# Optimization experiments

Hardware: AMD Instinct MI355X
Metric: run time of the kernel (lower is better)

The kernel has to match this reference:

```python
import math
import jax, jax.numpy as jnp
import numpy as np

B, T, C = 4, 2048, 1024
H = 16
D = C // H  # head dim = 64


def setup_inputs() -> dict:
    key = jax.random.key(0)
    ks = jax.random.split(key, 9)
    s = 0.02
    return {
        "x": jax.random.normal(ks[0], (B, T, C), dtype=jnp.float32),
        "Wq": jax.random.normal(ks[1], (C, C), dtype=jnp.float32) * s,
        "bq": jax.random.normal(ks[2], (C,), dtype=jnp.float32) * s,
        "Wk": jax.random.normal(ks[3], (C, C), dtype=jnp.float32) * s,
        "bk": jax.random.normal(ks[4], (C,), dtype=jnp.float32) * s,
        "Wv": jax.random.normal(ks[5], (C, C), dtype=jnp.float32) * s,
        "bv": jax.random.normal(ks[6], (C,), dtype=jnp.float32) * s,
        "Wo": jax.random.normal(ks[7], (C, C), dtype=jnp.float32) * s,
        "bo": jax.random.normal(ks[8], (C,), dtype=jnp.float32) * s,
    }


def reference(x, Wq, bq, Wk, bk, Wv, bv, Wo, bo):
    # Linear projections (torch Linear: x @ W.T + b), split into heads -> [B,H,T,D]
    def heads(y):
        return y.reshape(B, T, H, D).transpose(0, 2, 1, 3)

    q = heads(x @ Wq.T + bq)
    k = heads(x @ Wk.T + bk)
    v = heads(x @ Wv.T + bv)

    # Full [B,H,T,T] score matrix, scaled by 1/sqrt(D) (no mask, dropout=0 / eval)
    scores = jnp.einsum("bhqd,bhkd->bhqk", q, k) / math.sqrt(D)
    attn = jax.nn.softmax(scores, axis=-1)
    out = jnp.einsum("bhqk,bhkd->bhqd", attn, v)
    out = out.transpose(0, 2, 1, 3).reshape(B, T, C)
    return out @ Wo.T + bo
```

## Files before the change

kernel.cpp:

```cpp
#include <hip/hip_runtime.h>
#include <hip/hip_bf16.h>
#include <stdint.h>

#define Bb 4
#define Tt 2048
#define Cc 1024
#define Hh 16
#define Dd 64

using bf16x8 = __bf16 __attribute__((ext_vector_type(8)));
using f32x4  = float  __attribute__((ext_vector_type(4)));
using f32x2  = float  __attribute__((ext_vector_type(2)));
using f32x16 = float  __attribute__((ext_vector_type(16)));
typedef unsigned short u16;
typedef unsigned int   u32;

#if defined(__has_builtin) && __has_builtin(__builtin_amdgcn_exp2f)
#define EXP2F(x) __builtin_amdgcn_exp2f(x)
#else
#define EXP2F(x) exp2f(x)
#endif

#if defined(__has_builtin) && __has_builtin(__builtin_amdgcn_permlane32_swap)
#define PERMLANE32_SWAP(a, b)                                          \
  do {                                                                 \
    auto _r = __builtin_amdgcn_permlane32_swap((a), (b), false, false);\
    (a) = _r[0]; (b) = _r[1];                                          \
  } while (0)
#else
#define PERMLANE32_SWAP(a, b) \
  asm volatile("v_permlane32_swap_b32 %0, %1" : "+v"(a), "+v"(b))
#endif

__device__ __forceinline__ unsigned cvt_pk_bf16(float lo, float hi) {
  unsigned r;
  asm("v_cvt_pk_bf16_f32 %0, %1, %2" : "=v"(r) : "v"(lo), "v"(hi));
  return r;
}

__device__ __forceinline__ u16 f32_to_bf16(float f) {
  union { float f; unsigned u; } v; v.f = f;
  unsigned r = v.u + 0x7fffu + ((v.u >> 16) & 1u);
  return (u16)(r >> 16);
}

__device__ __forceinline__ void gl2lds16(const u16* g, u16* l) {
  __builtin_amdgcn_global_load_lds(
      (const __attribute__((address_space(1))) u32*)g,
      (__attribute__((address_space(3))) u32*)l, 16, 0, 0);
}

__global__ void cast_f32_to_bf16(const float* __restrict__ in, u16* __restrict__ out, int n) {
  int i = (blockIdx.x * blockDim.x + threadIdx.x) * 4;
  if (i >= n) return;
  float4 v = *reinterpret_cast<const float4*>(in + i);
  ushort4 o;
  o.x = f32_to_bf16(v.x); o.y = f32_to_bf16(v.y);
  o.z = f32_to_bf16(v.z); o.w = f32_to_bf16(v.w);
  *reinterpret_cast<ushort4*>(out + i) = o;
}

__global__ void cast4_f32_to_bf16(const float* __restrict__ w0, const float* __restrict__ w1,
                                  const float* __restrict__ w2, const float* __restrict__ w3,
                                  u16* __restrict__ o0, u16* __restrict__ o1,
                                  u16* __restrict__ o2, u16* __restrict__ o3, int n) {
  const float* in; u16* out;
  switch (blockIdx.y) {
    case 0: in = w0; out = o0; break;
    case 1: in = w1; out = o1; break;
    case 2: in = w2; out = o2; break;
    default: in = w3; out = o3; break;
  }
  int i = (blockIdx.x * blockDim.x + threadIdx.x) * 4;
  if (i >= n) return;
  float4 v = *reinterpret_cast<const float4*>(in + i);
  ushort4 o;
  o.x = f32_to_bf16(v.x); o.y = f32_to_bf16(v.y);
  o.z = f32_to_bf16(v.z); o.w = f32_to_bf16(v.w);
  *reinterpret_cast<ushort4*>(out + i) = o;
}

__global__ __launch_bounds__(256, 2)
void gemm_qkv(const u16* __restrict__ A, const u16* __restrict__ Bqkv,
              const float* __restrict__ bq, const float* __restrict__ bk,
              const float* __restrict__ bv,
              u16* __restrict__ qout, u16* __restrict__ kout, u16* __restrict__ vtout,
              float qscl)
{
  constexpr int K = Cc, BK = 32, LDT = 136;
  __shared__ alignas(16) u16 smem[128 * LDT];
  u16* As = smem;
  u16* Bs = smem + 128 * BK;
  const int tid  = threadIdx.x;
  const int wave = tid >> 6, lane = tid & 63;
  const int row0 = blockIdx.x * 128, col0 = blockIdx.y * 128;
  const int seg  = col0 >> 10;
  const int wm = (wave & 1) * 64, wn = (wave >> 1) * 64;
  const int fr = lane & 15, fk = (lane >> 4) * 8;
  const int srow = lane >> 2, scol = (lane & 3) * 8;

  f32x4 acc[4][4] = {};

  for (int k0 = 0; k0 < K; k0 += BK) {
#pragma unroll
    for (int c = 0; c < 2; ++c) {
      int rg = (wave * 2 + c) * 16;
      gl2lds16(A    + (size_t)(row0 + rg + srow) * K + k0 + scol, &As[rg * BK]);
      gl2lds16(Bqkv + (size_t)(col0 + rg + srow) * K + k0 + scol, &Bs[rg * BK]);
    }
    __syncthreads();
    bf16x8 af[4], bf[4];
#pragma unroll
    for (int i = 0; i < 4; ++i) {
      af[i] = *reinterpret_cast<const bf16x8*>(&As[(wm + i * 16 + fr) * BK + fk]);
      bf[i] = *reinterpret_cast<const bf16x8*>(&Bs[(wn + i * 16 + fr) * BK + fk]);
    }
#pragma unroll
    for (int i = 0; i < 4; ++i)
#pragma unroll
      for (int j = 0; j < 4; ++j)
        acc[i][j] = __builtin_amdgcn_mfma_f32_16x16x32_bf16(af[i], bf[j], acc[i][j], 0, 0, 0);
    __syncthreads();
  }

  const float* bias = (seg == 0) ? bq : ((seg == 1) ? bk : bv);
  const float scale = (seg == 0) ? qscl : 1.0f;
  const int colL0 = col0 & 1023;

  if (seg < 2) {
    u16* outp = (seg == 0) ? qout : kout;
#pragma unroll
    for (int j = 0; j < 4; ++j) {
      int col = colL0 + wn + j * 16 + fr;
      float bvv = bias[col];
#pragma unroll
      for (int i = 0; i < 4; ++i) {
        int rowb = row0 + wm + i * 16 + (lane >> 4) * 4;
#pragma unroll
        for (int r = 0; r < 4; ++r)
          outp[(size_t)(rowb + r) * Cc + col] = f32_to_bf16((acc[i][j][r] + bvv) * scale);
      }
    }
  } else {
#pragma unroll
    for (int j = 0; j < 4; ++j) {
      int lc = wn + j * 16 + fr;
      float bvv = bias[colL0 + lc];
#pragma unroll
      for (int i = 0; i < 4; ++i) {
        int lr = wm + i * 16 + (lane >> 4) * 4;
#pragma unroll
        for (int r = 0; r < 4; ++r)
          smem[lc * LDT + lr + r] = f32_to_bf16(acc[i][j][r] + bvv);
      }
    }
    __syncthreads();
    int lc = tid >> 1, seg2 = tid & 1;
    int col = colL0 + lc;
    int h = col >> 6, d = col & 63;
    int bb = row0 >> 11, t0 = (row0 & 2047) + seg2 * 64;
    u16* dst = vtout + ((size_t)(bb * Hh + h) * Dd + d) * Tt + t0;
    const u16* src = &smem[lc * LDT + seg2 * 64];
#pragma unroll
    for (int g = 0; g < 8; ++g)
      *reinterpret_cast<uint4*>(dst + g * 8) = *reinterpret_cast<const uint4*>(src + g * 8);
  }
}

__global__ __launch_bounds__(256, 2)
void gemm_out(const u16* __restrict__ A, const u16* __restrict__ Bw,
              const float* __restrict__ bias, float* __restrict__ Cout,
              int M, int N, int K)
{
  constexpr int BK = 32;
  __shared__ alignas(16) u16 As[128 * BK];
  __shared__ alignas(16) u16 Bs[128 * BK];
  const int tid  = threadIdx.x;
  const int wave = tid >> 6, lane = tid & 63;
  const int row0 = blockIdx.x * 128, col0 = blockIdx.y * 128;
  const int wm = (wave & 1) * 64, wn = (wave >> 1) * 64;
  const int fr = lane & 15, fk = (lane >> 4) * 8;
  const int srow = lane >> 2, scol = (lane & 3) * 8;

  f32x4 acc[4][4] = {};

  for (int k0 = 0; k0 < K; k0 += BK) {
#pragma unroll
    for (int c = 0; c < 2; ++c) {
      int rg = (wave * 2 + c) * 16;
      gl2lds16(A  + (size_t)(row0 + rg + srow) * K + k0 + scol, &As[rg * BK]);
      gl2lds16(Bw + (size_t)(col0 + rg + srow) * K + k0 + scol, &Bs[rg * BK]);
    }
    __syncthreads();
    bf16x8 af[4], bf[4];
#pragma unroll
    for (int i = 0; i < 4; ++i) {
      af[i] = *reinterpret_cast<const bf16x8*>(&As[(wm + i * 16 + fr) * BK + fk]);
      bf[i] = *reinterpret_cast<const bf16x8*>(&Bs[(wn + i * 16 + fr) * BK + fk]);
    }
#pragma unroll
    for (int i = 0; i < 4; ++i)
#pragma unroll
      for (int j = 0; j < 4; ++j)
        acc[i][j] = __builtin_amdgcn_mfma_f32_16x16x32_bf16(af[i], bf[j], acc[i][j], 0, 0, 0);
    __syncthreads();
  }

#pragma unroll
  for (int j = 0; j < 4; ++j) {
    int col = col0 + wn + j * 16 + fr;
    float bv = bias[col];
#pragma unroll
    for (int i = 0; i < 4; ++i) {
      int rowb = row0 + wm + i * 16 + (lane >> 4) * 4;
#pragma unroll
      for (int r = 0; r < 4; ++r)
        Cout[(size_t)(rowb + r) * N + col] = acc[i][j][r] + bv;
    }
  }
}

__global__ __launch_bounds__(256, 4)
void attn_kernel(const u16* __restrict__ Q, const u16* __restrict__ Kmat,
                 const u16* __restrict__ VT, u16* __restrict__ O) {
  __shared__ alignas(16) unsigned char smem[32768];
  float* OfT = (float*)smem;
  float* Qs  = (float*)(smem + 17408);

  const int tid = threadIdx.x, wave = tid >> 6, lane = tid & 63;
  const int l31 = lane & 31, hi = lane >> 5;
  const int qt = wave >> 1, kh = wave & 1;
  const int bh = blockIdx.x, qt0 = blockIdx.y;
  const int b = bh >> 4, h = bh & 15;
  const size_t base = (size_t)b * Tt * Cc + (size_t)h * Dd;
  const size_t vtb = (size_t)bh * Dd * Tt;

  bf16x8 qb[4];
  {
    const u16* qp = Q + base + (size_t)(qt0 * 64 + qt * 32 + l31) * Cc + hi * 8;
#pragma unroll
    for (int c = 0; c < 4; ++c)
      qb[c] = *reinterpret_cast<const bf16x8*>(qp + c * 16);
  }

  f32x16 Oacc[2] = {};
  f32x2 sacc = {0.f, 0.f};

  const u16* pK = Kmat + base + (size_t)(wave * 16 + (lane >> 3)) * Cc +
                  (((lane & 7) ^ (lane >> 3)) << 3);
  const u16* pV = VT + vtb + (size_t)(wave * 16 + (lane >> 3)) * Tt +
                  (((lane & 7) ^ (lane >> 3)) << 3);

  auto STAGE = [&](int buf, int kt) {
    u16* Kd = (u16*)(smem + (buf << 14)) + wave * 1024;
    u16* Vd = Kd + 4096;
    const u16* pk = pK + (size_t)kt * Cc;
    const u16* pv = pV + kt;
#pragma unroll
    for (int c = 0; c < 2; ++c) {
      gl2lds16(pk + (size_t)(c * 8) * Cc, Kd + c * 512);
      gl2lds16(pv + (size_t)(c * 8) * Tt, Vd + c * 512);
    }
  };

  STAGE(0, 0);
  __syncthreads();

  int cur = 0;
#pragma unroll 1
  for (int t = 0; t < 32; ++t) {
    if (t < 31) STAGE(cur ^ 1, (t + 1) << 6);

    const u16* Ks = (const u16*)(smem + (cur << 14));
    const u16* Vs = Ks + 4096;

    bf16x8 ka[4], vb[2][2];
    const int key = kh * 32 + l31;
#pragma unroll
    for (int c = 0; c < 4; ++c)
      ka[c] = *reinterpret_cast<const bf16x8*>(
          &Ks[key * 64 + ((((c << 1) + hi) ^ (key & 7)) << 3)]);
#pragma unroll
    for (int k0i = 0; k0i < 2; ++k0i)
#pragma unroll
      for (int dh = 0; dh < 2; ++dh) {
        int drow = dh * 32 + l31;
        int ch = kh * 4 + k0i * 2 + hi;
        vb[k0i][dh] = *reinterpret_cast<const bf16x8*>(
            &Vs[drow * 64 + ((ch ^ (drow & 7)) << 3)]);
      }

    __builtin_amdgcn_s_setprio(1);

    f32x16 s = {};
#pragma unroll
    for (int c = 0; c < 4; ++c)
      s = __builtin_amdgcn_mfma_f32_32x32x16_bf16(ka[c], qb[c], s, 0, 0, 0);
    unsigned pk8[8];
#pragma unroll
    for (int i = 0; i < 8; ++i) {
      float p0 = EXP2F(s[2 * i]), p1 = EXP2F(s[2 * i + 1]);
      sacc += (f32x2){p0, p1};
      pk8[i] = cvt_pk_bf16(p0, p1);
    }
    unsigned a0 = pk8[0], a1 = pk8[1], a2 = pk8[2], a3 = pk8[3];
    unsigned b0 = pk8[4], b1 = pk8[5], b2 = pk8[6], b3 = pk8[7];
    PERMLANE32_SWAP(a0, a2);
    PERMLANE32_SWAP(a1, a3);
    PERMLANE32_SWAP(b0, b2);
    PERMLANE32_SWAP(b1, b3);
    union { unsigned u[4]; bf16x8 v; } plo, phi;
    plo.u[0] = a0; plo.u[1] = a1; plo.u[2] = a2; plo.u[3] = a3;
    phi.u[0] = b0; phi.u[1] = b1; phi.u[2] = b2; phi.u[3] = b3;
    Oacc[0] = __builtin_amdgcn_mfma_f32_32x32x16_bf16(plo.v, vb[0][0], Oacc[0], 0, 0, 0);
    Oacc[1] = __builtin_amdgcn_mfma_f32_32x32x16_bf16(plo.v, vb[0][1], Oacc[1], 0, 0, 0);
    Oacc[0] = __builtin_amdgcn_mfma_f32_32x32x16_bf16(phi.v, vb[1][0], Oacc[0], 0, 0, 0);
    Oacc[1] = __builtin_amdgcn_mfma_f32_32x32x16_bf16(phi.v, vb[1][1], Oacc[1], 0, 0, 0);

    __builtin_amdgcn_s_setprio(0);

    __syncthreads();
    cur ^= 1;
  }

  {
    float s = sacc[0] + sacc[1];
    s += __shfl_xor(s, 32, 64);
    if (hi == 0) Qs[wave * 32 + l31] = s;
  }

#pragma unroll
  for (int step = 0; step < 2; ++step) {
    if (kh == step) {
#pragma unroll
      for (int dh = 0; dh < 2; ++dh) {
        int d = dh * 32 + l31;
        float* rowp = &OfT[d * 68 + qt * 32 + hi * 4];
#pragma unroll
        for (int g = 0; g < 4; ++g) {
          f32x4 v;
          v[0] = Oacc[dh][g * 4 + 0]; v[1] = Oacc[dh][g * 4 + 1];
          v[2] = Oacc[dh][g * 4 + 2]; v[3] = Oacc[dh][g * 4 + 3];
          float* dst = rowp + g * 8;
          if (step == 0) *reinterpret_cast<f32x4*>(dst) = v;
          else {
            f32x4 old = *reinterpret_cast<const f32x4*>(dst);
            *reinterpret_cast<f32x4*>(dst) = old + v;
          }
        }
      }
    }
    __syncthreads();
  }

  {
    int q = tid >> 2, dg = tid & 3;
    float qtot = Qs[(q >> 5) * 64 + (q & 31)] + Qs[(q >> 5) * 64 + 32 + (q & 31)];
    float linv = 1.0f / qtot;
    alignas(16) u16 tmp[16];
#pragma unroll
    for (int i = 0; i < 16; ++i)
      tmp[i] = f32_to_bf16(OfT[(dg * 16 + i) * 68 + q] * linv);
    u16* op = O + base + (size_t)(qt0 * 64 + q) * Cc + dg * 16;
    *reinterpret_cast<uint4*>(op)     = *reinterpret_cast<const uint4*>(tmp);
    *reinterpret_cast<uint4*>(op + 8) = *reinterpret_cast<const uint4*>(tmp + 8);
  }
}

extern "C" void kernel_launch(void* const* d_in, const int* in_sizes, int n_in,
                              void* d_out, int out_size, void* d_ws, size_t ws_size,
                              hipStream_t stream) {
  const float* x  = (const float*)d_in[0];
  const float* Wq = (const float*)d_in[1];
  const float* bq = (const float*)d_in[2];
  const float* Wk = (const float*)d_in[3];
  const float* bk = (const float*)d_in[4];
  const float* Wv = (const float*)d_in[5];
  const float* bv = (const float*)d_in[6];
  const float* Wo = (const float*)d_in[7];
  const float* bo = (const float*)d_in[8];

  const size_t NX = (size_t)Bb * Tt * Cc;
  const size_t NW = (size_t)Cc * Cc;

  u16* ws  = (u16*)d_ws;
  u16* xb  = ws;
  u16* wqb = ws + NX;
  u16* wkb = wqb + NW;
  u16* wvb = wkb + NW;
  u16* wob = wvb + NW;
  u16* qb  = wob + NW;
  u16* kb  = qb + NX;
  u16* vtb = kb + NX;
  u16* attnb = xb;

  cast_f32_to_bf16<<<(int)(NX / 4 / 256), 256, 0, stream>>>(x, xb, (int)NX);
  cast4_f32_to_bf16<<<dim3((unsigned)(NW / 4 / 256), 4), 256, 0, stream>>>(
      Wq, Wk, Wv, Wo, wqb, wkb, wvb, wob, (int)NW);

  const float QSCL = 0.125f * 1.44269504f;
  gemm_qkv<<<dim3(64, 24), 256, 0, stream>>>(xb, wqb, bq, bk, bv, qb, kb, vtb, QSCL);

  attn_kernel<<<dim3(Bb * Hh, Tt / 64), 256, 0, stream>>>(qb, kb, vtb, attnb);

  gemm_out<<<dim3(64, 8), 256, 0, stream>>>(attnb, wob, bo, (float*)d_out,
                                            Bb * Tt, Cc, Cc);
}
```

Before: 291.2 us.

## Load K/V tiles directly from global into registers, drop LDS staging, swizzle blocks

The attention kernel no longer stages K and V tiles through double-buffered shared memory with per-iteration barriers. Each wave now reads its K and V fragments straight from global memory into registers, and K loads are software-prefetched one tile ahead. The launch becomes a 1D grid with a block-index swizzle so that neighbouring blocks share the same head, which should improve L2 reuse, and shared memory shrinks. The trade-off is that each wave issues its own, possibly less coalesced global loads, and the two waves sharing keys read duplicate data, so the kernel relies on the cache hierarchy instead of LDS.

```diff
diff --git a/kernel.cpp b/kernel.cpp
--- a/kernel.cpp
+++ b/kernel.cpp
@@ -223,14 +223,16 @@
 __global__ __launch_bounds__(256, 4)
 void attn_kernel(const u16* __restrict__ Q, const u16* __restrict__ Kmat,
                  const u16* __restrict__ VT, u16* __restrict__ O) {
-  __shared__ alignas(16) unsigned char smem[32768];
+  __shared__ alignas(16) unsigned char smem[18432];
   float* OfT = (float*)smem;
   float* Qs  = (float*)(smem + 17408);
 
   const int tid = threadIdx.x, wave = tid >> 6, lane = tid & 63;
   const int l31 = lane & 31, hi = lane >> 5;
   const int qt = wave >> 1, kh = wave & 1;
-  const int bh = blockIdx.x, qt0 = blockIdx.y;
+  const int flat = blockIdx.x;
+  const int swz = (flat & 7) * 256 + (flat >> 3);
+  const int bh = swz >> 5, qt0 = swz & 31;
   const int b = bh >> 4, h = bh & 15;
   const size_t base = (size_t)b * Tt * Cc + (size_t)h * Dd;
   const size_t vtb = (size_t)bh * Dd * Tt;
@@ -246,82 +248,70 @@
   f32x16 Oacc[2] = {};
   f32x2 sacc = {0.f, 0.f};
 
-  const u16* pK = Kmat + base + (size_t)(wave * 16 + (lane >> 3)) * Cc +
-                  (((lane & 7) ^ (lane >> 3)) << 3);
-  const u16* pV = VT + vtb + (size_t)(wave * 16 + (lane >> 3)) * Tt +
-                  (((lane & 7) ^ (lane >> 3)) << 3);
-
-  auto STAGE = [&](int buf, int kt) {
-    u16* Kd = (u16*)(smem + (buf << 14)) + wave * 1024;
-    u16* Vd = Kd + 4096;
-    const u16* pk = pK + (size_t)kt * Cc;
-    const u16* pv = pV + kt;
-#pragma unroll
-    for (int c = 0; c < 2; ++c) {
-      gl2lds16(pk + (size_t)(c * 8) * Cc, Kd + c * 512);
-      gl2lds16(pv + (size_t)(c * 8) * Tt, Vd + c * 512);
-    }
-  };
-
-  STAGE(0, 0);
+  const int koff  = (kh * 32 + l31) * Cc + hi * 8;
+  const int voff0 = l31 * Tt        + kh * 32 + hi * 8;
+  const int voff1 = (32 + l31) * Tt + kh * 32 + hi * 8;
+  const u16* kp = Kmat + base;
+  const u16* vp = VT + vtb;
+
+#define LOADK(T, KA)                                                       \
+  {                                                                        \
+    const u16* kpt = kp + (size_t)(T) * 64 * Cc + koff;                    \
+    KA[0] = *reinterpret_cast<const bf16x8*>(kpt);                         \
+    KA[1] = *reinterpret_cast<const bf16x8*>(kpt + 16);                    \
+    KA[2] = *reinterpret_cast<const bf16x8*>(kpt + 32);                    \
+    KA[3] = *reinterpret_cast<const bf16x8*>(kpt + 48);                    \
+  }
+
+#define BODY(T, KA)                                                        \
+  {                                                                        \
+    const u16* vpt = vp + (T) * 64;                                        \
+    bf16x8 vb00 = *reinterpret_cast<const bf16x8*>(vpt + voff0);           \
+    bf16x8 vb10 = *reinterpret_cast<const bf16x8*>(vpt + voff0 + 16);      \
+    bf16x8 vb01 = *reinterpret_cast<const bf16x8*>(vpt + voff1);           \
+    bf16x8 vb11 = *reinterpret_cast<const bf16x8*>(vpt + voff1 + 16);      \
+    __builtin_amdgcn_s_setprio(1);                                         \
+    f32x16 s = {};                                                         \
+    s = __builtin_amdgcn_mfma_f32_32x32x16_bf16(KA[0], qb[0], s, 0, 0, 0); \
+    s = __builtin_amdgcn_mfma_f32_32x32x16_bf16(KA[1], qb[1], s, 0, 0, 0); \
+    s = __builtin_amdgcn_mfma_f32_32x32x16_bf16(KA[2], qb[2], s, 0, 0, 0); \
+    s = __builtin_amdgcn_mfma_f32_32x32x16_bf16(KA[3], qb[3], s, 0, 0, 0); \
+    unsigned pk8[8];                                                       \
+    _Pragma("unroll")                                                      \
+    for (int i = 0; i < 8; ++i) {                                          \
+      float p0 = EXP2F(s[2 * i]), p1 = EXP2F(s[2 * i + 1]);                \
+      sacc += (f32x2){p0, p1};                                             \
+      pk8[i] = cvt_pk_bf16(p0, p1);                                        \
+    }                                                                      \
+    unsigned a0 = pk8[0], a1 = pk8[1], a2 = pk8[2], a3 = pk8[3];           \
+    unsigned b0 = pk8[4], b1 = pk8[5], b2 = pk8[6], b3 = pk8[7];           \
+    PERMLANE32_SWAP(a0, a2);                                               \
+    PERMLANE32_SWAP(a1, a3);                                               \
+    PERMLANE32_SWAP(b0, b2);                                               \
+    PERMLANE32_SWAP(b1, b3);                                               \
+    union { unsigned u[4]; bf16x8 v; } plo, phi;                           \
+    plo.u[0] = a0; plo.u[1] = a1; plo.u[2] = a2; plo.u[3] = a3;            \
+    phi.u[0] = b0; phi.u[1] = b1; phi.u[2] = b2; phi.u[3] = b3;            \
+    Oacc[0] = __builtin_amdgcn_mfma_f32_32x32x16_bf16(plo.v, vb00, Oacc[0], 0, 0, 0); \
+    Oacc[1] = __builtin_amdgcn_mfma_f32_32x32x16_bf16(plo.v, vb01, Oacc[1], 0, 0, 0); \
+    Oacc[0] = __builtin_amdgcn_mfma_f32_32x32x16_bf16(phi.v, vb10, Oacc[0], 0, 0, 0); \
+    Oacc[1] = __builtin_amdgcn_mfma_f32_32x32x16_bf16(phi.v, vb11, Oacc[1], 0, 0, 0); \
+    __builtin_amdgcn_s_setprio(0);                                         \
+  }
+
+  bf16x8 ka0[4], ka1[4];
+  LOADK(0, ka0);
+#pragma unroll 1
+  for (int t = 0; t < 32; t += 2) {
+    LOADK(t + 1, ka1);
+    BODY(t, ka0);
+    if (t < 30) LOADK(t + 2, ka0);
+    BODY(t + 1, ka1);
+  }
+#undef LOADK
+#undef BODY
+
   __syncthreads();
-
-  int cur = 0;
-#pragma unroll 1
-  for (int t = 0; t < 32; ++t) {
-    if (t < 31) STAGE(cur ^ 1, (t + 1) << 6);
-
-    const u16* Ks = (const u16*)(smem + (cur << 14));
-    const u16* Vs = Ks + 4096;
-
-    bf16x8 ka[4], vb[2][2];
-    const int key = kh * 32 + l31;
-#pragma unroll
-    for (int c = 0; c < 4; ++c)
-      ka[c] = *reinterpret_cast<const bf16x8*>(
-          &Ks[key * 64 + ((((c << 1) + hi) ^ (key & 7)) << 3)]);
-#pragma unroll
-    for (int k0i = 0; k0i < 2; ++k0i)
-#pragma unroll
-      for (int dh = 0; dh < 2; ++dh) {
-        int drow = dh * 32 + l31;
-        int ch = kh * 4 + k0i * 2 + hi;
-        vb[k0i][dh] = *reinterpret_cast<const bf16x8*>(
-            &Vs[drow * 64 + ((ch ^ (drow & 7)) << 3)]);
-      }
-
-    __builtin_amdgcn_s_setprio(1);
-
-    f32x16 s = {};
-#pragma unroll
-    for (int c = 0; c < 4; ++c)
-      s = __builtin_amdgcn_mfma_f32_32x32x16_bf16(ka[c], qb[c], s, 0, 0, 0);
-    unsigned pk8[8];
-#pragma unroll
-    for (int i = 0; i < 8; ++i) {
-      float p0 = EXP2F(s[2 * i]), p1 = EXP2F(s[2 * i + 1]);
-      sacc += (f32x2){p0, p1};
-      pk8[i] = cvt_pk_bf16(p0, p1);
-    }
-    unsigned a0 = pk8[0], a1 = pk8[1], a2 = pk8[2], a3 = pk8[3];
-    unsigned b0 = pk8[4], b1 = pk8[5], b2 = pk8[6], b3 = pk8[7];
-    PERMLANE32_SWAP(a0, a2);
-    PERMLANE32_SWAP(a1, a3);
-    PERMLANE32_SWAP(b0, b2);
-    PERMLANE32_SWAP(b1, b3);
-    union { unsigned u[4]; bf16x8 v; } plo, phi;
-    plo.u[0] = a0; plo.u[1] = a1; plo.u[2] = a2; plo.u[3] = a3;
-    phi.u[0] = b0; phi.u[1] = b1; phi.u[2] = b2; phi.u[3] = b3;
-    Oacc[0] = __builtin_amdgcn_mfma_f32_32x32x16_bf16(plo.v, vb[0][0], Oacc[0], 0, 0, 0);
-    Oacc[1] = __builtin_amdgcn_mfma_f32_32x32x16_bf16(plo.v, vb[0][1], Oacc[1], 0, 0, 0);
-    Oacc[0] = __builtin_amdgcn_mfma_f32_32x32x16_bf16(phi.v, vb[1][0], Oacc[0], 0, 0, 0);
-    Oacc[1] = __builtin_amdgcn_mfma_f32_32x32x16_bf16(phi.v, vb[1][1], Oacc[1], 0, 0, 0);
-
-    __builtin_amdgcn_s_setprio(0);
-
-    __syncthreads();
-    cur ^= 1;
-  }
 
   {
     float s = sacc[0] + sacc[1];
@@ -401,7 +391,7 @@
   const float QSCL = 0.125f * 1.44269504f;
   gemm_qkv<<<dim3(64, 24), 256, 0, stream>>>(xb, wqb, bq, bk, bv, qb, kb, vtb, QSCL);
 
-  attn_kernel<<<dim3(Bb * Hh, Tt / 64), 256, 0, stream>>>(qb, kb, vtb, attnb);
+  attn_kernel<<<dim3(Bb * Hh * (Tt / 64)), 256, 0, stream>>>(qb, kb, vtb, attnb);
 
   gemm_out<<<dim3(64, 8), 256, 0, stream>>>(attnb, wob, bo, (float*)d_out,
                                             Bb * Tt, Cc, Cc);
```

New measurement: 435.7 us. +49.6%, slower.

## Deepen GEMM K-tile to 64 with XOR-swizzled LDS and XCD-aware block mapping

Applied to the files above, without the earlier changes.

Both projection GEMMs now stage K-tiles of 64 instead of 32, halving the number of barrier pairs per output tile. The LDS layout is XOR-swizzled on 16-byte chunks to avoid bank conflicts on the fragment reads. The grid becomes 1D and is remapped so that consecutive blocks on the same XCD cover neighbouring row tiles, improving L2 reuse. The QKV kernel gains an extra barrier before reusing shared memory for the V transpose. LDS use per block doubles in gemm_out.

```diff
diff --git a/kernel.cpp b/kernel.cpp
--- a/kernel.cpp
+++ b/kernel.cpp
@@ -87,39 +87,51 @@
               u16* __restrict__ qout, u16* __restrict__ kout, u16* __restrict__ vtout,
               float qscl)
 {
-  constexpr int K = Cc, BK = 32, LDT = 136;
+  constexpr int K = Cc, BK = 64, LDT = 136;
   __shared__ alignas(16) u16 smem[128 * LDT];
   u16* As = smem;
-  u16* Bs = smem + 128 * BK;
+  u16* Bs = smem + 128 * 64;
   const int tid  = threadIdx.x;
   const int wave = tid >> 6, lane = tid & 63;
-  const int row0 = blockIdx.x * 128, col0 = blockIdx.y * 128;
+  const int lid = blockIdx.x;
+  const int xcd = lid & 7, cch = lid >> 3;
+  const int bx = xcd * 8 + (cch & 7), by = cch >> 3;
+  const int row0 = bx * 128, col0 = by * 128;
   const int seg  = col0 >> 10;
   const int wm = (wave & 1) * 64, wn = (wave >> 1) * 64;
-  const int fr = lane & 15, fk = (lane >> 4) * 8;
-  const int srow = lane >> 2, scol = (lane & 3) * 8;
+  const int fr = lane & 15, qd = lane >> 4;
+  const int srow = lane >> 3;
+  const int scol = ((lane & 7) ^ srow) << 3;
 
   f32x4 acc[4][4] = {};
+  const u16* pA = A    + (size_t)(row0 + wave * 32 + srow) * K + scol;
+  const u16* pB = Bqkv + (size_t)(col0 + wave * 32 + srow) * K + scol;
 
   for (int k0 = 0; k0 < K; k0 += BK) {
 #pragma unroll
-    for (int c = 0; c < 2; ++c) {
-      int rg = (wave * 2 + c) * 16;
-      gl2lds16(A    + (size_t)(row0 + rg + srow) * K + k0 + scol, &As[rg * BK]);
-      gl2lds16(Bqkv + (size_t)(col0 + rg + srow) * K + k0 + scol, &Bs[rg * BK]);
-    }
-    __syncthreads();
-    bf16x8 af[4], bf[4];
-#pragma unroll
-    for (int i = 0; i < 4; ++i) {
-      af[i] = *reinterpret_cast<const bf16x8*>(&As[(wm + i * 16 + fr) * BK + fk]);
-      bf[i] = *reinterpret_cast<const bf16x8*>(&Bs[(wn + i * 16 + fr) * BK + fk]);
-    }
-#pragma unroll
-    for (int i = 0; i < 4; ++i)
-#pragma unroll
-      for (int j = 0; j < 4; ++j)
-        acc[i][j] = __builtin_amdgcn_mfma_f32_16x16x32_bf16(af[i], bf[j], acc[i][j], 0, 0, 0);
+    for (int c = 0; c < 4; ++c) {
+      gl2lds16(pA + (size_t)(c * 8) * K + k0, &As[(wave * 32 + c * 8) * 64]);
+      gl2lds16(pB + (size_t)(c * 8) * K + k0, &Bs[(wave * 32 + c * 8) * 64]);
+    }
+    __syncthreads();
+#pragma unroll
+    for (int kk = 0; kk < 2; ++kk) {
+      bf16x8 af[4], bf[4];
+#pragma unroll
+      for (int i = 0; i < 4; ++i) {
+        int ra = wm + i * 16 + fr;
+        af[i] = *reinterpret_cast<const bf16x8*>(
+            &As[ra * 64 + (((kk * 4 + qd) ^ (ra & 7)) << 3)]);
+        int rb = wn + i * 16 + fr;
+        bf[i] = *reinterpret_cast<const bf16x8*>(
+            &Bs[rb * 64 + (((kk * 4 + qd) ^ (rb & 7)) << 3)]);
+      }
+#pragma unroll
+      for (int i = 0; i < 4; ++i)
+#pragma unroll
+        for (int j = 0; j < 4; ++j)
+          acc[i][j] = __builtin_amdgcn_mfma_f32_16x16x32_bf16(af[i], bf[j], acc[i][j], 0, 0, 0);
+    }
     __syncthreads();
   }
 
@@ -142,6 +154,7 @@
       }
     }
   } else {
+    __syncthreads();
 #pragma unroll
     for (int j = 0; j < 4; ++j) {
       int lc = wn + j * 16 + fr;
@@ -172,37 +185,49 @@
               const float* __restrict__ bias, float* __restrict__ Cout,
               int M, int N, int K)
 {
-  constexpr int BK = 32;
-  __shared__ alignas(16) u16 As[128 * BK];
-  __shared__ alignas(16) u16 Bs[128 * BK];
+  constexpr int BK = 64;
+  __shared__ alignas(16) u16 As[128 * 64];
+  __shared__ alignas(16) u16 Bs[128 * 64];
   const int tid  = threadIdx.x;
   const int wave = tid >> 6, lane = tid & 63;
-  const int row0 = blockIdx.x * 128, col0 = blockIdx.y * 128;
+  const int lid = blockIdx.x;
+  const int xcd = lid & 7, cch = lid >> 3;
+  const int bx = xcd * 8 + (cch & 7), by = cch >> 3;
+  const int row0 = bx * 128, col0 = by * 128;
   const int wm = (wave & 1) * 64, wn = (wave >> 1) * 64;
-  const int fr = lane & 15, fk = (lane >> 4) * 8;
-  const int srow = lane >> 2, scol = (lane & 3) * 8;
+  const int fr = lane & 15, qd = lane >> 4;
+  const int srow = lane >> 3;
+  const int scol = ((lane & 7) ^ srow) << 3;
 
   f32x4 acc[4][4] = {};
+  const u16* pA = A  + (size_t)(row0 + wave * 32 + srow) * K + scol;
+  const u16* pB = Bw + (size_t)(col0 + wave * 32 + srow) * K + scol;
 
   for (int k0 = 0; k0 < K; k0 += BK) {
 #pragma unroll
-    for (int c = 0; c < 2; ++c) {
-      int rg = (wave * 2 + c) * 16;
-      gl2lds16(A  + (size_t)(row0 + rg + srow) * K + k0 + scol, &As[rg * BK]);
-      gl2lds16(Bw + (size_t)(col0 + rg + srow) * K + k0 + scol, &Bs[rg * BK]);
-    }
-    __syncthreads();
-    bf16x8 af[4], bf[4];
-#pragma unroll
-    for (int i = 0; i < 4; ++i) {
-      af[i] = *reinterpret_cast<const bf16x8*>(&As[(wm + i * 16 + fr) * BK + fk]);
-      bf[i] = *reinterpret_cast<const bf16x8*>(&Bs[(wn + i * 16 + fr) * BK + fk]);
-    }
-#pragma unroll
-    for (int i = 0; i < 4; ++i)
-#pragma unroll
-      for (int j = 0; j < 4; ++j)
-        acc[i][j] = __builtin_amdgcn_mfma_f32_16x16x32_bf16(af[i], bf[j], acc[i][j], 0, 0, 0);
+    for (int c = 0; c < 4; ++c) {
+      gl2lds16(pA + (size_t)(c * 8) * K + k0, &As[(wave * 32 + c * 8) * 64]);
+      gl2lds16(pB + (size_t)(c * 8) * K + k0, &Bs[(wave * 32 + c * 8) * 64]);
+    }
+    __syncthreads();
+#pragma unroll
+    for (int kk = 0; kk < 2; ++kk) {
+      bf16x8 af[4], bf[4];
+#pragma unroll
+      for (int i = 0; i < 4; ++i) {
+        int ra = wm + i * 16 + fr;
+        af[i] = *reinterpret_cast<const bf16x8*>(
+            &As[ra * 64 + (((kk * 4 + qd) ^ (ra & 7)) << 3)]);
+        int rb = wn + i * 16 + fr;
+        bf[i] = *reinterpret_cast<const bf16x8*>(
+            &Bs[rb * 64 + (((kk * 4 + qd) ^ (rb & 7)) << 3)]);
+      }
+#pragma unroll
+      for (int i = 0; i < 4; ++i)
+#pragma unroll
+        for (int j = 0; j < 4; ++j)
+          acc[i][j] = __builtin_amdgcn_mfma_f32_16x16x32_bf16(af[i], bf[j], acc[i][j], 0, 0, 0);
+    }
     __syncthreads();
   }
 
@@ -399,10 +424,10 @@
       Wq, Wk, Wv, Wo, wqb, wkb, wvb, wob, (int)NW);
 
   const float QSCL = 0.125f * 1.44269504f;
-  gemm_qkv<<<dim3(64, 24), 256, 0, stream>>>(xb, wqb, bq, bk, bv, qb, kb, vtb, QSCL);
+  gemm_qkv<<<dim3(1536), 256, 0, stream>>>(xb, wqb, bq, bk, bv, qb, kb, vtb, QSCL);
 
   attn_kernel<<<dim3(Bb * Hh, Tt / 64), 256, 0, stream>>>(qb, kb, vtb, attnb);
 
-  gemm_out<<<dim3(64, 8), 256, 0, stream>>>(attnb, wob, bo, (float*)d_out,
-                                            Bb * Tt, Cc, Cc);
-}
+  gemm_out<<<dim3(512), 256, 0, stream>>>(attnb, wob, bo, (float*)d_out,
+                                          Bb * Tt, Cc, Cc);
+}
```

New measurement: 271.3 us. 1.07x faster.

## Replace GEMMs with double-buffered 256x128 swizzled-LDS pipelined kernel and fuse casts

Applied to the files above, without the earlier changes.

Both projection GEMMs now use one kernel with 512 threads, 256x128 tiles, BK=64, XOR-swizzled LDS, and double-buffered global-to-LDS loads. Loads are interleaved with MFMA phases and gated by s_waitcnt, with setprio and an XCD-aware block remap. The two cast kernels are merged into one launch. The aim is to hide global-load latency and cut the per-tile barrier stalls of the old single-buffered 128x128 GEMMs. The cost is more LDS per block (96KB), which limits occupancy, plus fragile hand-written waitcnt/barrier scheduling.

```diff
diff --git a/kernel.cpp b/kernel.cpp
--- a/kernel.cpp
+++ b/kernel.cpp
@@ -50,173 +50,178 @@
       (__attribute__((address_space(3))) u32*)l, 16, 0, 0);
 }
 
-__global__ void cast_f32_to_bf16(const float* __restrict__ in, u16* __restrict__ out, int n) {
-  int i = (blockIdx.x * blockDim.x + threadIdx.x) * 4;
-  if (i >= n) return;
-  float4 v = *reinterpret_cast<const float4*>(in + i);
+__global__ void cast_all(const float* __restrict__ x,
+                         const float* __restrict__ w0, const float* __restrict__ w1,
+                         const float* __restrict__ w2, const float* __restrict__ w3,
+                         u16* __restrict__ out) {
+  size_t e = ((size_t)blockIdx.x * blockDim.x + threadIdx.x) * 4;
+  size_t hi = e >> 20;
+  const float* src;
+  if (hi < 8) {
+    src = x + e;
+  } else {
+    size_t off = e & 1048575u;
+    src = (hi == 8 ? w0 : hi == 9 ? w1 : hi == 10 ? w2 : w3) + off;
+  }
+  float4 v = *reinterpret_cast<const float4*>(src);
   ushort4 o;
   o.x = f32_to_bf16(v.x); o.y = f32_to_bf16(v.y);
   o.z = f32_to_bf16(v.z); o.w = f32_to_bf16(v.w);
-  *reinterpret_cast<ushort4*>(out + i) = o;
-}
-
-__global__ void cast4_f32_to_bf16(const float* __restrict__ w0, const float* __restrict__ w1,
-                                  const float* __restrict__ w2, const float* __restrict__ w3,
-                                  u16* __restrict__ o0, u16* __restrict__ o1,
-                                  u16* __restrict__ o2, u16* __restrict__ o3, int n) {
-  const float* in; u16* out;
-  switch (blockIdx.y) {
-    case 0: in = w0; out = o0; break;
-    case 1: in = w1; out = o1; break;
-    case 2: in = w2; out = o2; break;
-    default: in = w3; out = o3; break;
-  }
-  int i = (blockIdx.x * blockDim.x + threadIdx.x) * 4;
-  if (i >= n) return;
-  float4 v = *reinterpret_cast<const float4*>(in + i);
-  ushort4 o;
-  o.x = f32_to_bf16(v.x); o.y = f32_to_bf16(v.y);
-  o.z = f32_to_bf16(v.z); o.w = f32_to_bf16(v.w);
-  *reinterpret_cast<ushort4*>(out + i) = o;
-}
-
-__global__ __launch_bounds__(256, 2)
-void gemm_qkv(const u16* __restrict__ A, const u16* __restrict__ Bqkv,
-              const float* __restrict__ bq, const float* __restrict__ bk,
-              const float* __restrict__ bv,
-              u16* __restrict__ qout, u16* __restrict__ kout, u16* __restrict__ vtout,
-              float qscl)
+  *reinterpret_cast<ushort4*>(out + e) = o;
+}
+
+__global__ __launch_bounds__(512, 2)
+void gemm8(const u16* __restrict__ A, const u16* __restrict__ Bm,
+           const float* __restrict__ b0, const float* __restrict__ b1,
+           const float* __restrict__ b2,
+           u16* __restrict__ o0, u16* __restrict__ o1, u16* __restrict__ vtout,
+           float* __restrict__ of32, float qscl, int isqkv)
 {
-  constexpr int K = Cc, BK = 32, LDT = 136;
-  __shared__ alignas(16) u16 smem[128 * LDT];
-  u16* As = smem;
-  u16* Bs = smem + 128 * BK;
-  const int tid  = threadIdx.x;
+  constexpr int K = Cc;
+  __shared__ alignas(16) u16 smem16[49152];
+  const int tid = threadIdx.x;
   const int wave = tid >> 6, lane = tid & 63;
-  const int row0 = blockIdx.x * 128, col0 = blockIdx.y * 128;
-  const int seg  = col0 >> 10;
-  const int wm = (wave & 1) * 64, wn = (wave >> 1) * 64;
-  const int fr = lane & 15, fk = (lane >> 4) * 8;
-  const int srow = lane >> 2, scol = (lane & 3) * 8;
+  const int fr = lane & 15, qd = lane >> 4, sw = fr & 7;
+  const int wr = wave >> 1, wc = wave & 1;
+  const int lid = blockIdx.x;
+  const int xcd = lid & 7, idx = lid >> 3;
+  const int bx = xcd * 4 + (idx & 3), by = idx >> 2;
+  const int row0 = bx * 256, col0 = by * 128;
+
+  const u16* pA = A  + (size_t)(row0 + (lane >> 3)) * K + (((lane & 7) ^ (lane >> 3)) << 3);
+  const u16* pB = Bm + (size_t)(col0 + (lane >> 3)) * K + (((lane & 7) ^ (lane >> 3)) << 3);
 
   f32x4 acc[4][4] = {};
-
-  for (int k0 = 0; k0 < K; k0 += BK) {
-#pragma unroll
-    for (int c = 0; c < 2; ++c) {
-      int rg = (wave * 2 + c) * 16;
-      gl2lds16(A    + (size_t)(row0 + rg + srow) * K + k0 + scol, &As[rg * BK]);
-      gl2lds16(Bqkv + (size_t)(col0 + rg + srow) * K + k0 + scol, &Bs[rg * BK]);
+  bf16x8 bfr[4][2];
+
+#define STG_A(BUF, H, T) do {                                              \
+    gl2lds16(pA + (size_t)((H)*128 + wave*16) * K + (T)*64,                \
+             smem16 + (BUF)*24576 + ((H)*128 + wave*16) * 64);             \
+    gl2lds16(pA + (size_t)((H)*128 + wave*16 + 8) * K + (T)*64,            \
+             smem16 + (BUF)*24576 + ((H)*128 + wave*16 + 8) * 64);         \
+  } while (0)
+#define STG_B(BUF, T) do {                                                 \
+    gl2lds16(pB + (size_t)(wave*16) * K + (T)*64,                          \
+             smem16 + (BUF)*24576 + 16384 + (wave*16) * 64);               \
+    gl2lds16(pB + (size_t)(wave*16 + 8) * K + (T)*64,                      \
+             smem16 + (BUF)*24576 + 16384 + (wave*16 + 8) * 64);           \
+  } while (0)
+#define LDA(BUF, Q, KK) (*reinterpret_cast<const bf16x8*>(                 \
+    &smem16[(BUF)*24576 + (wr*64 + (Q)*16 + fr) * 64 + ((((KK)*4 + qd) ^ sw) << 3)]))
+#define LDB(BUF, J, KK) (*reinterpret_cast<const bf16x8*>(                 \
+    &smem16[(BUF)*24576 + 16384 + (wc*64 + (J)*16 + fr) * 64 + ((((KK)*4 + qd) ^ sw) << 3)]))
+#define GATE2 asm volatile("s_waitcnt vmcnt(2)" ::: "memory")
+#define GATE0 asm volatile("s_waitcnt vmcnt(0)" ::: "memory")
+#define GNONE
+#define SBAR do { asm volatile("" ::: "memory");                           \
+    __builtin_amdgcn_s_barrier(); asm volatile("" ::: "memory"); } while (0)
+
+#define PH(Q, BUF, GATE, ...) do {                                         \
+    bf16x8 af0 = LDA(BUF, Q, 0), af1 = LDA(BUF, Q, 1);                     \
+    if ((Q) == 0) {                                                        \
+      bfr[0][0] = LDB(BUF, 0, 0); bfr[0][1] = LDB(BUF, 0, 1);              \
+      bfr[1][0] = LDB(BUF, 1, 0); bfr[1][1] = LDB(BUF, 1, 1);              \
+      bfr[2][0] = LDB(BUF, 2, 0); bfr[2][1] = LDB(BUF, 2, 1);              \
+      bfr[3][0] = LDB(BUF, 3, 0); bfr[3][1] = LDB(BUF, 3, 1);              \
+    }                                                                      \
+    __VA_ARGS__;                                                           \
+    asm volatile("" ::: "memory");                                         \
+    __builtin_amdgcn_s_barrier();                                          \
+    asm volatile("s_waitcnt lgkmcnt(0)" ::: "memory");                     \
+    __builtin_amdgcn_sched_barrier(0);                                     \
+    __builtin_amdgcn_s_setprio(1);                                         \
+    acc[Q][0] = __builtin_amdgcn_mfma_f32_16x16x32_bf16(af0, bfr[0][0], acc[Q][0], 0, 0, 0); \
+    acc[Q][0] = __builtin_amdgcn_mfma_f32_16x16x32_bf16(af1, bfr[0][1], acc[Q][0], 0, 0, 0); \
+    acc[Q][1] = __builtin_amdgcn_mfma_f32_16x16x32_bf16(af0, bfr[1][0], acc[Q][1], 0, 0, 0); \
+    acc[Q][1] = __builtin_amdgcn_mfma_f32_16x16x32_bf16(af1, bfr[1][1], acc[Q][1], 0, 0, 0); \
+    acc[Q][2] = __builtin_amdgcn_mfma_f32_16x16x32_bf16(af0, bfr[2][0], acc[Q][2], 0, 0, 0); \
+    acc[Q][2] = __builtin_amdgcn_mfma_f32_16x16x32_bf16(af1, bfr[2][1], acc[Q][2], 0, 0, 0); \
+    acc[Q][3] = __builtin_amdgcn_mfma_f32_16x16x32_bf16(af0, bfr[3][0], acc[Q][3], 0, 0, 0); \
+    acc[Q][3] = __builtin_amdgcn_mfma_f32_16x16x32_bf16(af1, bfr[3][1], acc[Q][3], 0, 0, 0); \
+    __builtin_amdgcn_s_setprio(0);                                         \
+    GATE;                                                                  \
+    SBAR;                                                                  \
+  } while (0)
+
+  STG_B(0, 0); STG_A(0, 0, 0); STG_A(0, 1, 0); STG_B(1, 1);
+  GATE2;
+  SBAR;
+
+#pragma unroll 1
+  for (int i = 0; i < 8; ++i) {
+    const int t1 = 2 * i + 1, t2 = 2 * i + 2, t3 = 2 * i + 3;
+    const bool g = i < 7;
+    PH(0, 0, GNONE, STG_A(1, 0, t1));
+    PH(1, 0, GNONE, STG_A(1, 1, t1));
+    PH(2, 0, GNONE, if (g) STG_B(0, t2));
+    if (g) { PH(3, 0, GATE2, ); } else { PH(3, 0, GATE0, ); }
+    PH(0, 1, GNONE, if (g) STG_A(0, 0, t2));
+    PH(1, 1, GNONE, if (g) STG_A(0, 1, t2));
+    PH(2, 1, GNONE, if (g) STG_B(1, t3));
+    PH(3, 1, GATE2, );
+  }
+#undef PH
+#undef STG_A
+#undef STG_B
+#undef LDA
+#undef LDB
+
+  const int colL0 = col0 & 1023;
+  if (!isqkv) {
+#pragma unroll
+    for (int j = 0; j < 4; ++j) {
+      int col = col0 + wc * 64 + j * 16 + fr;
+      float bv = b0[col];
+#pragma unroll
+      for (int m = 0; m < 4; ++m) {
+        int rowb = row0 + wr * 64 + m * 16 + qd * 4;
+#pragma unroll
+        for (int r = 0; r < 4; ++r)
+          of32[(size_t)(rowb + r) * Cc + col] = acc[m][j][r] + bv;
+      }
+    }
+    return;
+  }
+  const int seg = col0 >> 10;
+  const float* bias = (seg == 0) ? b0 : ((seg == 1) ? b1 : b2);
+  const float scale = (seg == 0) ? qscl : 1.0f;
+  if (seg < 2) {
+    u16* outp = (seg == 0) ? o0 : o1;
+#pragma unroll
+    for (int j = 0; j < 4; ++j) {
+      int col = colL0 + wc * 64 + j * 16 + fr;
+      float bv = bias[col];
+#pragma unroll
+      for (int m = 0; m < 4; ++m) {
+        int rowb = row0 + wr * 64 + m * 16 + qd * 4;
+#pragma unroll
+        for (int r = 0; r < 4; ++r)
+          outp[(size_t)(rowb + r) * Cc + col] = f32_to_bf16((acc[m][j][r] + bv) * scale);
+      }
+    }
+  } else {
+#pragma unroll
+    for (int j = 0; j < 4; ++j) {
+      int lc = wc * 64 + j * 16 + fr;
+      float bv = bias[colL0 + lc];
+#pragma unroll
+      for (int m = 0; m < 4; ++m) {
+        int lr = wr * 64 + m * 16 + qd * 4;
+#pragma unroll
+        for (int r = 0; r < 4; ++r)
+          smem16[lc * 264 + lr + r] = f32_to_bf16(acc[m][j][r] + bv);
+      }
     }
     __syncthreads();
-    bf16x8 af[4], bf[4];
-#pragma unroll
-    for (int i = 0; i < 4; ++i) {
-      af[i] = *reinterpret_cast<const bf16x8*>(&As[(wm + i * 16 + fr) * BK + fk]);
-      bf[i] = *reinterpret_cast<const bf16x8*>(&Bs[(wn + i * 16 + fr) * BK + fk]);
-    }
-#pragma unroll
-    for (int i = 0; i < 4; ++i)
-#pragma unroll
-      for (int j = 0; j < 4; ++j)
-        acc[i][j] = __builtin_amdgcn_mfma_f32_16x16x32_bf16(af[i], bf[j], acc[i][j], 0, 0, 0);
-    __syncthreads();
-  }
-
-  const float* bias = (seg == 0) ? bq : ((seg == 1) ? bk : bv);
-  const float scale = (seg == 0) ? qscl : 1.0f;
-  const int colL0 = col0 & 1023;
-
-  if (seg < 2) {
-    u16* outp = (seg == 0) ? qout : kout;
-#pragma unroll
-    for (int j = 0; j < 4; ++j) {
-      int col = colL0 + wn + j * 16 + fr;
-      float bvv = bias[col];
-#pragma unroll
-      for (int i = 0; i < 4; ++i) {
-        int rowb = row0 + wm + i * 16 + (lane >> 4) * 4;
-#pragma unroll
-        for (int r = 0; r < 4; ++r)
-          outp[(size_t)(rowb + r) * Cc + col] = f32_to_bf16((acc[i][j][r] + bvv) * scale);
-      }
-    }
-  } else {
-#pragma unroll
-    for (int j = 0; j < 4; ++j) {
-      int lc = wn + j * 16 + fr;
-      float bvv = bias[colL0 + lc];
-#pragma unroll
-      for (int i = 0; i < 4; ++i) {
-        int lr = wm + i * 16 + (lane >> 4) * 4;
-#pragma unroll
-        for (int r = 0; r < 4; ++r)
-          smem[lc * LDT + lr + r] = f32_to_bf16(acc[i][j][r] + bvv);
-      }
-    }
-    __syncthreads();
-    int lc = tid >> 1, seg2 = tid & 1;
+    int lc = tid >> 2, quarter = tid & 3;
     int col = colL0 + lc;
     int h = col >> 6, d = col & 63;
-    int bb = row0 >> 11, t0 = (row0 & 2047) + seg2 * 64;
+    int bb = row0 >> 11, t0 = (row0 & 2047) + quarter * 64;
     u16* dst = vtout + ((size_t)(bb * Hh + h) * Dd + d) * Tt + t0;
-    const u16* src = &smem[lc * LDT + seg2 * 64];
-#pragma unroll
-    for (int g = 0; g < 8; ++g)
-      *reinterpret_cast<uint4*>(dst + g * 8) = *reinterpret_cast<const uint4*>(src + g * 8);
-  }
-}
-
-__global__ __launch_bounds__(256, 2)
-void gemm_out(const u16* __restrict__ A, const u16* __restrict__ Bw,
-              const float* __restrict__ bias, float* __restrict__ Cout,
-              int M, int N, int K)
-{
-  constexpr int BK = 32;
-  __shared__ alignas(16) u16 As[128 * BK];
-  __shared__ alignas(16) u16 Bs[128 * BK];
-  const int tid  = threadIdx.x;
-  const int wave = tid >> 6, lane = tid & 63;
-  const int row0 = blockIdx.x * 128, col0 = blockIdx.y * 128;
-  const int wm = (wave & 1) * 64, wn = (wave >> 1) * 64;
-  const int fr = lane & 15, fk = (lane >> 4) * 8;
-  const int srow = lane >> 2, scol = (lane & 3) * 8;
-
-  f32x4 acc[4][4] = {};
-
-  for (int k0 = 0; k0 < K; k0 += BK) {
-#pragma unroll
-    for (int c = 0; c < 2; ++c) {
-      int rg = (wave * 2 + c) * 16;
-      gl2lds16(A  + (size_t)(row0 + rg + srow) * K + k0 + scol, &As[rg * BK]);
-      gl2lds16(Bw + (size_t)(col0 + rg + srow) * K + k0 + scol, &Bs[rg * BK]);
-    }
-    __syncthreads();
-    bf16x8 af[4], bf[4];
-#pragma unroll
-    for (int i = 0; i < 4; ++i) {
-      af[i] = *reinterpret_cast<const bf16x8*>(&As[(wm + i * 16 + fr) * BK + fk]);
-      bf[i] = *reinterpret_cast<const bf16x8*>(&Bs[(wn + i * 16 + fr) * BK + fk]);
-    }
-#pragma unroll
-    for (int i = 0; i < 4; ++i)
-#pragma unroll
-      for (int j = 0; j < 4; ++j)
-        acc[i][j] = __builtin_amdgcn_mfma_f32_16x16x32_bf16(af[i], bf[j], acc[i][j], 0, 0, 0);
-    __syncthreads();
-  }
-
-#pragma unroll
-  for (int j = 0; j < 4; ++j) {
-    int col = col0 + wn + j * 16 + fr;
-    float bv = bias[col];
-#pragma unroll
-    for (int i = 0; i < 4; ++i) {
-      int rowb = row0 + wm + i * 16 + (lane >> 4) * 4;
-#pragma unroll
-      for (int r = 0; r < 4; ++r)
-        Cout[(size_t)(rowb + r) * N + col] = acc[i][j][r] + bv;
-    }
+    const u16* src = &smem16[lc * 264 + quarter * 64];
+#pragma unroll
+    for (int g2 = 0; g2 < 8; ++g2)
+      *reinterpret_cast<uint4*>(dst + g2 * 8) = *reinterpret_cast<const uint4*>(src + g2 * 8);
   }
 }
 
@@ -394,15 +399,15 @@
   u16* vtb = kb + NX;
   u16* attnb = xb;
 
-  cast_f32_to_bf16<<<(int)(NX / 4 / 256), 256, 0, stream>>>(x, xb, (int)NX);
-  cast4_f32_to_bf16<<<dim3((unsigned)(NW / 4 / 256), 4), 256, 0, stream>>>(
-      Wq, Wk, Wv, Wo, wqb, wkb, wvb, wob, (int)NW);
+  cast_all<<<dim3(12288), 256, 0, stream>>>(x, Wq, Wk, Wv, Wo, ws);
 
   const float QSCL = 0.125f * 1.44269504f;
-  gemm_qkv<<<dim3(64, 24), 256, 0, stream>>>(xb, wqb, bq, bk, bv, qb, kb, vtb, QSCL);
+  gemm8<<<dim3(768), 512, 0, stream>>>(xb, wqb, bq, bk, bv, qb, kb, vtb,
+                                       nullptr, QSCL, 1);
 
   attn_kernel<<<dim3(Bb * Hh, Tt / 64), 256, 0, stream>>>(qb, kb, vtb, attnb);
 
-  gemm_out<<<dim3(64, 8), 256, 0, stream>>>(attnb, wob, bo, (float*)d_out,
-                                            Bb * Tt, Cc, Cc);
-}
+  gemm8<<<dim3(256), 512, 0, stream>>>(attnb, wob, bo, nullptr, nullptr,
+                                       nullptr, nullptr, nullptr,
+                                       (float*)d_out, 1.0f, 0);
+}
```

After: 274.5 us. -5.7%, faster.
